# Optimization experiments

Hardware: AMD Instinct MI355X
Metric: run time of the kernel (lower is better)

Reference implementation:

```python
import jax, jax.numpy as jnp
import numpy as np

ALPHA = 1.0
BLOCK = 128  # row block size for the pairwise L1 reduction


def _pairwise_score(features, a):
    # score[i, j] = sum_k |f[i,k] - f[j,k]| * a[k]
    # computed in row blocks to avoid the O(n^2*d) broadcast intermediate
    n, d = features.shape
    av = a[:, 0]  # [d]
    fb = features.reshape(n // BLOCK, BLOCK, d)

    def blk(fblk):  # fblk: [B, d]
        diff = jnp.abs(fblk[:, None, :] - features[None, :, :])  # [B, n, d]
        return jnp.einsum('bnd,d->bn', diff, av)                  # [B, n]

    return jax.lax.map(blk, fb).reshape(n, n)


def setup_inputs() -> dict:
    key = jax.random.key(0)
    n, d = 8192, 256
    features = jax.random.normal(key, (n, d), dtype=jnp.float32)
    a = jnp.full((d, 1), 0.01, dtype=jnp.float32)  # nn.init.constant_(a, 0.01)
    return {"features": features, "a": a}


def reference(features, a):
    score = _pairwise_score(features, a)                 # [n, n]
    adjacency = jnp.exp(-ALPHA * jax.nn.relu(score))     # [n, n]
    # D^{-1/2} A D^{-1/2} via row/col elementwise scaling (== diag mm mm)
    dsq = jnp.sum(adjacency, axis=1) ** -0.5             # [n]
    normalized = dsq[:, None] * adjacency * dsq[None, :]
    return (normalized, adjacency)
```

## Files before the change

### kernel.cpp

```cpp
#include <hip/hip_runtime.h>
#include <math.h>

#define BM 128
#define BN 128
#define BK 32

typedef unsigned int uint;

__device__ __forceinline__ uint fenc(float f) {
    uint u = __float_as_uint(f);
    return (u & 0x80000000u) ? ~u : (u | 0x80000000u);
}
__device__ __forceinline__ float fdec(uint u) {
    uint v = (u & 0x80000000u) ? (u & 0x7FFFFFFFu) : ~u;
    return __uint_as_float(v);
}

__global__ __launch_bounds__(256) void init_kernel(uint* __restrict__ flags,
                                                   float* __restrict__ rowsum,
                                                   const float* __restrict__ A,
                                                   int n, int d, int zb)
{
    const int b = blockIdx.x, t = threadIdx.x;
    if (b < zb) { int i = b * 256 + t; if (i < n) rowsum[i] = 0.f; return; }
    if (t == 0) { flags[0] = 0u; flags[1] = 0xFFFFFFFFu; flags[2] = 0u; }
    __syncthreads();
    for (int k = t; k < d; k += 256)
        if (A[k] < 0.f) atomicOr(&flags[0], 1u);
}

__global__ __launch_bounds__(256) void minmax_kernel(const float* __restrict__ F,
                                                     const float* __restrict__ A,
                                                     uint* __restrict__ flags,
                                                     int n, int d)
{
    const int total4 = n * d / 4;
    float lmin = 3.4e38f, lmax = -3.4e38f;
    for (int e4 = blockIdx.x * 256 + threadIdx.x; e4 < total4; e4 += gridDim.x * 256) {
        int e = e4 * 4;
        int dk = e % d;
        float4 f = *(const float4*)(F + e);
        float4 a = *(const float4*)(A + dk);
        float g0 = fabsf(a.x) * f.x, g1 = fabsf(a.y) * f.y;
        float g2 = fabsf(a.z) * f.z, g3 = fabsf(a.w) * f.w;
        lmin = fminf(lmin, fminf(fminf(g0, g1), fminf(g2, g3)));
        lmax = fmaxf(lmax, fmaxf(fmaxf(g0, g1), fmaxf(g2, g3)));
    }
    #pragma unroll
    for (int m = 1; m < 64; m <<= 1) {
        lmin = fminf(lmin, __shfl_xor(lmin, m));
        lmax = fmaxf(lmax, __shfl_xor(lmax, m));
    }
    if ((threadIdx.x & 63) == 0) {
        atomicMin(&flags[1], fenc(lmin));
        atomicMax(&flags[2], fenc(lmax));
    }
}

__global__ __launch_bounds__(256) void quant_kernel(const float* __restrict__ F,
                                                    const float* __restrict__ A,
                                                    const uint* __restrict__ flags,
                                                    uint* __restrict__ Q,
                                                    int n, int d)
{
    const int t = threadIdx.x;
    const int r = blockIdx.x * 32 + (t & 31);
    const int kqb = t >> 5;
    const int d4 = d >> 2;
    const float gmin = fdec(flags[1]), gmax = fdec(flags[2]);
    const float span = gmax - gmin;
    const float inv = span > 0.f ? 255.f / span : 0.f;
    for (int kq = kqb; kq < d4; kq += 8) {
        float4 f = *(const float4*)(F + (size_t)r * d + kq * 4);
        float4 a = *(const float4*)(A + kq * 4);
        uint q0 = 0, q1 = 0, q2 = 0, q3 = 0;
        if (a.x > 0.f) q0 = (uint)fminf(fmaxf((a.x * f.x - gmin) * inv + 0.5f, 0.f), 255.f);
        if (a.y > 0.f) q1 = (uint)fminf(fmaxf((a.y * f.y - gmin) * inv + 0.5f, 0.f), 255.f);
        if (a.z > 0.f) q2 = (uint)fminf(fmaxf((a.z * f.z - gmin) * inv + 0.5f, 0.f), 255.f);
        if (a.w > 0.f) q3 = (uint)fminf(fmaxf((a.w * f.w - gmin) * inv + 0.5f, 0.f), 255.f);
        Q[(size_t)kq * n + r] = q0 | (q1 << 8) | (q2 << 16) | (q3 << 24);
    }
}

__global__ __launch_bounds__(256) void adj_sad_kernel(const uint* __restrict__ Q,
                                                      const uint* __restrict__ flags,
                                                      float* __restrict__ adj,
                                                      float* __restrict__ rowsum,
                                                      int n, int d)
{
    if (flags[0] != 0u) return;

    __shared__ uint As[16][128];
    __shared__ uint Bs[16][128];

    const int t = threadIdx.x, tx = t & 15, ty = t >> 4;
    const int i0 = blockIdx.y * 128, j0 = blockIdx.x * 128;
    const int d4 = d >> 2, chunks = d4 >> 4;

    const float gmin = fdec(flags[1]), gmax = fdec(flags[2]);
    const float step = (gmax - gmin) * (1.f / 255.f);

    uint acc[8][8] = {};

    const int kk0 = t >> 5;
    const int col = 4 * (t & 31);

    uint4 sa[2], sb[2];
    #pragma unroll
    for (int j = 0; j < 2; ++j) {
        size_t g = ((size_t)(kk0 + 8 * j)) * n;
        sa[j] = *(const uint4*)(Q + g + i0 + col);
        sb[j] = *(const uint4*)(Q + g + j0 + col);
    }

    for (int c = 0; c < chunks; ++c) {
        ((uint4*)&As[0][0])[t]       = sa[0];
        ((uint4*)&As[0][0])[256 + t] = sa[1];
        ((uint4*)&Bs[0][0])[t]       = sb[0];
        ((uint4*)&Bs[0][0])[256 + t] = sb[1];
        __syncthreads();

        if (c + 1 < chunks) {
            #pragma unroll
            for (int j = 0; j < 2; ++j) {
                size_t g = ((size_t)((c + 1) * 16 + kk0 + 8 * j)) * n;
                sa[j] = *(const uint4*)(Q + g + i0 + col);
                sb[j] = *(const uint4*)(Q + g + j0 + col);
            }
        }

        #pragma unroll
        for (int kk = 0; kk < 16; ++kk) {
            uint ar[8], br[8];
            *(uint4*)&ar[0] = *(const uint4*)&As[kk][4 * ty];
            *(uint4*)&ar[4] = *(const uint4*)&As[kk][64 + 4 * ty];
            *(uint4*)&br[0] = *(const uint4*)&Bs[kk][4 * tx];
            *(uint4*)&br[4] = *(const uint4*)&Bs[kk][64 + 4 * tx];
            #pragma unroll
            for (int m = 0; m < 8; ++m)
                #pragma unroll
                for (int cc = 0; cc < 8; ++cc)
                    acc[m][cc] = __builtin_amdgcn_sad_u8(ar[m], br[cc], acc[m][cc]);
        }
        __syncthreads();
    }

    #pragma unroll
    for (int m = 0; m < 8; ++m) {
        const int row = i0 + (m >> 2) * 64 + 4 * ty + (m & 3);
        float rs = 0.f;
        #pragma unroll
        for (int qh = 0; qh < 2; ++qh) {
            float4 v;
            v.x = __expf(-fmaxf(step * (float)acc[m][qh * 4 + 0], 0.f));
            v.y = __expf(-fmaxf(step * (float)acc[m][qh * 4 + 1], 0.f));
            v.z = __expf(-fmaxf(step * (float)acc[m][qh * 4 + 2], 0.f));
            v.w = __expf(-fmaxf(step * (float)acc[m][qh * 4 + 3], 0.f));
            rs += (v.x + v.y) + (v.z + v.w);
            *(float4*)(adj + (size_t)row * n + j0 + qh * 64 + 4 * tx) = v;
        }
        rs += __shfl_xor(rs, 1);
        rs += __shfl_xor(rs, 2);
        rs += __shfl_xor(rs, 4);
        rs += __shfl_xor(rs, 8);
        if (tx == 0) atomicAdd(rowsum + row, rs);
    }
}

__global__ __launch_bounds__(256) void adj_kernel(
    const float* __restrict__ F, const float* __restrict__ A,
    const uint* __restrict__ flags,
    float* __restrict__ adj, float* __restrict__ rowsum, int n, int d)
{
    if (flags[0] == 0u) return;

    __shared__ __align__(16) float As[BK][BM + 4];
    __shared__ __align__(16) float Bs[BK][BN + 4];
    __shared__ float aw[256];

    const int t  = threadIdx.x;
    const int tx = t & 15;
    const int ty = t >> 4;
    const int i0 = blockIdx.y * BM;
    const int j0 = blockIdx.x * BN;

    for (int k = t; k < d; k += 256) aw[k] = A[k];

    float acc[2][2][4][4] = {};

    const int lr = t >> 3;
    const int lk = (t & 7) << 2;

    for (int kc = 0; kc < d; kc += BK) {
        __syncthreads();
        #pragma unroll
        for (int s = 0; s < 4; ++s) {
            int r = lr + 32 * s;
            float4 v = *(const float4*)(F + (size_t)(i0 + r) * d + kc + lk);
            As[lk + 0][r] = v.x; As[lk + 1][r] = v.y;
            As[lk + 2][r] = v.z; As[lk + 3][r] = v.w;
            float4 u = *(const float4*)(F + (size_t)(j0 + r) * d + kc + lk);
            Bs[lk + 0][r] = u.x; Bs[lk + 1][r] = u.y;
            Bs[lk + 2][r] = u.z; Bs[lk + 3][r] = u.w;
        }
        __syncthreads();

        #pragma unroll
        for (int k = 0; k < BK; ++k) {
            float av[2][4], bv[2][4];
            *(float4*)&av[0][0] = *(const float4*)&As[k][4 * ty];
            *(float4*)&av[1][0] = *(const float4*)&As[k][64 + 4 * ty];
            *(float4*)&bv[0][0] = *(const float4*)&Bs[k][4 * tx];
            *(float4*)&bv[1][0] = *(const float4*)&Bs[k][64 + 4 * tx];
            const float w = aw[kc + k];
            #pragma unroll
            for (int p = 0; p < 2; ++p)
                #pragma unroll
                for (int m = 0; m < 4; ++m)
                    #pragma unroll
                    for (int q = 0; q < 2; ++q)
                        #pragma unroll
                        for (int c = 0; c < 4; ++c)
                            acc[p][q][m][c] += fabsf(av[p][m] - bv[q][c]) * w;
        }
    }

    #pragma unroll
    for (int p = 0; p < 2; ++p) {
        #pragma unroll
        for (int m = 0; m < 4; ++m) {
            const int row = i0 + p * 64 + ty * 4 + m;
            float rs = 0.f;
            #pragma unroll
            for (int q = 0; q < 2; ++q) {
                float4 v;
                v.x = __expf(-fmaxf(acc[p][q][m][0], 0.f));
                v.y = __expf(-fmaxf(acc[p][q][m][1], 0.f));
                v.z = __expf(-fmaxf(acc[p][q][m][2], 0.f));
                v.w = __expf(-fmaxf(acc[p][q][m][3], 0.f));
                rs += (v.x + v.y) + (v.z + v.w);
                *(float4*)(adj + (size_t)row * n + j0 + q * 64 + tx * 4) = v;
            }
            rs += __shfl_xor(rs, 1);
            rs += __shfl_xor(rs, 2);
            rs += __shfl_xor(rs, 4);
            rs += __shfl_xor(rs, 8);
            if (tx == 0) atomicAdd(rowsum + row, rs);
        }
    }
}

__global__ __launch_bounds__(256) void dsq_kernel(
    const float* __restrict__ rowsum, float* __restrict__ dsq, int n)
{
    int i = blockIdx.x * 256 + threadIdx.x;
    if (i < n) dsq[i] = 1.f / sqrtf(rowsum[i]);
}

__global__ __launch_bounds__(256) void norm_kernel(
    const float* __restrict__ adj, const float* __restrict__ dsq,
    float* __restrict__ out, int n)
{
    const int i = blockIdx.y;
    const int j = (blockIdx.x * 256 + threadIdx.x) * 4;
    if (j >= n) return;
    const float di = dsq[i];
    float4 a = *(const float4*)(adj + (size_t)i * n + j);
    float4 dj = *(const float4*)(dsq + j);
    float4 o;
    o.x = di * a.x * dj.x;
    o.y = di * a.y * dj.y;
    o.z = di * a.z * dj.z;
    o.w = di * a.w * dj.w;
    *(float4*)(out + (size_t)i * n + j) = o;
}

extern "C" void kernel_launch(void* const* d_in, const int* in_sizes, int n_in,
                              void* d_out, int out_size, void* d_ws, size_t ws_size,
                              hipStream_t stream)
{
    const float* F = (const float*)d_in[0];
    const float* A = (const float*)d_in[1];
    const int d = in_sizes[1];
    const int n = in_sizes[0] / d;

    float* out    = (float*)d_out;
    float* adj    = out + (size_t)n * n;
    uint*  flags  = (uint*)d_ws;
    float* rowsum = (float*)d_ws + 8;
    float* dsq    = rowsum + n;
    uint* Q = (uint*)d_out;

    const int zb = (n + 255) / 256;
    init_kernel<<<dim3(zb + 1), dim3(256), 0, stream>>>(flags, rowsum, A, n, d, zb);
    minmax_kernel<<<dim3(256), dim3(256), 0, stream>>>(F, A, flags, n, d);
    quant_kernel<<<dim3(n / 32), dim3(256), 0, stream>>>(F, A, flags, Q, n, d);

    dim3 gridA(n / 128, n / 128);
    adj_sad_kernel<<<gridA, dim3(256), 0, stream>>>(Q, flags, adj, rowsum, n, d);
    adj_kernel<<<gridA, dim3(256), 0, stream>>>(F, A, flags, adj, rowsum, n, d);

    dsq_kernel<<<dim3((n + 255) / 256), dim3(256), 0, stream>>>(rowsum, dsq, n);

    dim3 gridN(n / 1024, n);
    norm_kernel<<<gridN, dim3(256), 0, stream>>>(adj, dsq, out, n);
}
```

Baseline: 325.7 us.

## Exploit score symmetry: compute upper-triangular tiles and mirror-write transposed blocks

The quantized SAD kernel now launches only the upper-triangular set of 128x128 tiles. It decodes tile coordinates from a linear block index, and each off-diagonal tile writes both its block and the transposed block, adding column sums to rowsum with atomics. This roughly halves the SAD compute, at the cost of strided transposed stores and extra atomics. Separately, the normalize kernel makes each thread handle four float4 chunks, and launch bounds request 3 blocks per SIMD-level occupancy.

Measured after the change: 323.6 us. No clear change (-0.7%).

```diff
diff --git a/kernel.cpp b/kernel.cpp
--- a/kernel.cpp
+++ b/kernel.cpp
@@ -82,19 +82,27 @@
     }
 }
 
-__global__ __launch_bounds__(256) void adj_sad_kernel(const uint* __restrict__ Q,
-                                                      const uint* __restrict__ flags,
-                                                      float* __restrict__ adj,
-                                                      float* __restrict__ rowsum,
-                                                      int n, int d)
+__global__ __launch_bounds__(256, 3) void adj_sad_kernel(const uint* __restrict__ Q,
+                                                         const uint* __restrict__ flags,
+                                                         float* __restrict__ adj,
+                                                         float* __restrict__ rowsum,
+                                                         int n, int d)
 {
     if (flags[0] != 0u) return;
 
     __shared__ uint As[16][128];
     __shared__ uint Bs[16][128];
 
+    int b = blockIdx.x;
+    int bx = (int)((sqrtf(8.f * (float)b + 1.f) - 1.f) * 0.5f);
+    while ((bx + 1) * (bx + 2) / 2 <= b) ++bx;
+    while (bx * (bx + 1) / 2 > b) --bx;
+    const int by = b - bx * (bx + 1) / 2;
+
     const int t = threadIdx.x, tx = t & 15, ty = t >> 4;
-    const int i0 = blockIdx.y * 128, j0 = blockIdx.x * 128;
+    const int i0 = by * 128;
+    const int j0 = bx * 128;
+    const bool diag = (bx == by);
     const int d4 = d >> 2, chunks = d4 >> 4;
 
     const float gmin = fdec(flags[1]), gmax = fdec(flags[2]);
@@ -145,17 +153,21 @@
         __syncthreads();
     }
 
+    float e[8][8];
+    #pragma unroll
+    for (int m = 0; m < 8; ++m)
+        #pragma unroll
+        for (int cc = 0; cc < 8; ++cc)
+            e[m][cc] = __expf(-step * (float)acc[m][cc]);
+
     #pragma unroll
     for (int m = 0; m < 8; ++m) {
         const int row = i0 + (m >> 2) * 64 + 4 * ty + (m & 3);
         float rs = 0.f;
         #pragma unroll
         for (int qh = 0; qh < 2; ++qh) {
-            float4 v;
-            v.x = __expf(-fmaxf(step * (float)acc[m][qh * 4 + 0], 0.f));
-            v.y = __expf(-fmaxf(step * (float)acc[m][qh * 4 + 1], 0.f));
-            v.z = __expf(-fmaxf(step * (float)acc[m][qh * 4 + 2], 0.f));
-            v.w = __expf(-fmaxf(step * (float)acc[m][qh * 4 + 3], 0.f));
+            float4 v = make_float4(e[m][qh * 4 + 0], e[m][qh * 4 + 1],
+                                   e[m][qh * 4 + 2], e[m][qh * 4 + 3]);
             rs += (v.x + v.y) + (v.z + v.w);
             *(float4*)(adj + (size_t)row * n + j0 + qh * 64 + 4 * tx) = v;
         }
@@ -164,6 +176,40 @@
         rs += __shfl_xor(rs, 4);
         rs += __shfl_xor(rs, 8);
         if (tx == 0) atomicAdd(rowsum + row, rs);
+    }
+
+    if (!diag) {
+        #pragma unroll
+        for (int h = 0; h < 2; ++h)
+            #pragma unroll
+            for (int qh = 0; qh < 2; ++qh)
+                #pragma unroll
+                for (int cc = 0; cc < 4; ++cc) {
+                    float4 v = make_float4(e[4 * h + 0][qh * 4 + cc],
+                                           e[4 * h + 1][qh * 4 + cc],
+                                           e[4 * h + 2][qh * 4 + cc],
+                                           e[4 * h + 3][qh * 4 + cc]);
+                    const int r = j0 + qh * 64 + 4 * tx + cc;
+                    *(float4*)(adj + (size_t)r * n + i0 + 64 * h + 4 * ty) = v;
+                }
+
+        float cs[8];
+        #pragma unroll
+        for (int cc = 0; cc < 8; ++cc) {
+            float s = 0.f;
+            #pragma unroll
+            for (int m = 0; m < 8; ++m) s += e[m][cc];
+            s += __shfl_xor(s, 16);
+            s += __shfl_xor(s, 32);
+            cs[cc] = s;
+        }
+        if ((t & 48) == 0) {
+            #pragma unroll
+            for (int qh = 0; qh < 2; ++qh)
+                #pragma unroll
+                for (int cc = 0; cc < 4; ++cc)
+                    atomicAdd(rowsum + j0 + qh * 64 + 4 * tx + cc, cs[qh * 4 + cc]);
+        }
     }
 }
 
@@ -262,17 +308,21 @@
     float* __restrict__ out, int n)
 {
     const int i = blockIdx.y;
-    const int j = (blockIdx.x * 256 + threadIdx.x) * 4;
-    if (j >= n) return;
     const float di = dsq[i];
-    float4 a = *(const float4*)(adj + (size_t)i * n + j);
-    float4 dj = *(const float4*)(dsq + j);
-    float4 o;
-    o.x = di * a.x * dj.x;
-    o.y = di * a.y * dj.y;
-    o.z = di * a.z * dj.z;
-    o.w = di * a.w * dj.w;
-    *(float4*)(out + (size_t)i * n + j) = o;
+    const int base = blockIdx.x * 4096;
+    #pragma unroll
+    for (int k = 0; k < 4; ++k) {
+        const int j = base + k * 1024 + threadIdx.x * 4;
+        if (j >= n) return;
+        float4 a = *(const float4*)(adj + (size_t)i * n + j);
+        float4 dj = *(const float4*)(dsq + j);
+        float4 o;
+        o.x = di * a.x * dj.x;
+        o.y = di * a.y * dj.y;
+        o.z = di * a.z * dj.z;
+        o.w = di * a.w * dj.w;
+        *(float4*)(out + (size_t)i * n + j) = o;
+    }
 }
 
 extern "C" void kernel_launch(void* const* d_in, const int* in_sizes, int n_in,
@@ -296,12 +346,13 @@
     minmax_kernel<<<dim3(256), dim3(256), 0, stream>>>(F, A, flags, n, d);
     quant_kernel<<<dim3(n / 32), dim3(256), 0, stream>>>(F, A, flags, Q, n, d);
 
-    dim3 gridA(n / 128, n / 128);
-    adj_sad_kernel<<<gridA, dim3(256), 0, stream>>>(Q, flags, adj, rowsum, n, d);
-    adj_kernel<<<gridA, dim3(256), 0, stream>>>(F, A, flags, adj, rowsum, n, d);
+    const int nb = n / 128;
+    const int tri = nb * (nb + 1) / 2;
+    adj_sad_kernel<<<dim3(tri), dim3(256), 0, stream>>>(Q, flags, adj, rowsum, n, d);
+    adj_kernel<<<dim3(nb, nb), dim3(256), 0, stream>>>(F, A, flags, adj, rowsum, n, d);
 
     dsq_kernel<<<dim3((n + 255) / 256), dim3(256), 0, stream>>>(rowsum, dsq, n);
 
-    dim3 gridN(n / 1024, n);
+    dim3 gridN((n + 4095) / 4096, n);
     norm_kernel<<<gridN, dim3(256), 0, stream>>>(adj, dsq, out, n);
 }
```
